# Kernel optimization log

Measured on AMD Instinct MI355X. Metric: run time of the kernel, lower is better.

Reference implementation:

```python
import jax, jax.numpy as jnp
import numpy as np
from jax import lax

B, H, W, C, G, K = 2, 64, 64, 256, 8, 9
CQ = C // 4  # PConv partial channels
HC = C // G  # head channels
PTS = np.array([[-1, -1], [-1, 0], [-1, 1], [0, -1], [0, 0], [0, 1],
                [1, -1], [1, 0], [1, 1]], np.float32)  # (K,2) as (dx,dy)


def setup_inputs() -> dict:
    key = jax.random.key(0)
    ks = jax.random.split(key, 13)
    n = lambda i, shp, s: jax.random.normal(ks[i], shp, jnp.float32) * s
    return {
        'x': jax.random.normal(ks[0], (B, H, W, C), jnp.float32),
        'qkv_w': n(1, (C, 3 * C), C ** -0.5),
        'qkv_b': n(2, (3 * C,), 0.02),
        'dw_w': n(3, (3, 3, 1, 3 * C), 1.0 / 3.0),
        'dw_b': n(4, (3 * C,), 0.02),
        'off_pconv_w': n(5, (G, CQ, CQ, 3, 3), (CQ * 9) ** -0.5),
        'off_w': n(6, (G, 2 * K, C), 0.1 * C ** -0.5),
        'off_b': n(7, (G, 2 * K), 0.1),
        'mask_pconv_w': n(8, (CQ, CQ, 3, 3), (CQ * 9) ** -0.5),
        'mask_w': n(9, (K, C), C ** -0.5),
        'mask_b': n(10, (K,), 0.02),
        'proj_w': n(11, (C, C), C ** -0.5),
        'proj_b': n(12, (C,), 0.02),
    }


def _dwconv_nhwc(x, w, b):
    # depthwise 3x3, pad 1, stride 1; x (B,H,W,ch), w (3,3,1,ch)
    ch = x.shape[-1]
    y = lax.conv_general_dilated(x, w, (1, 1), 'SAME',
                                 dimension_numbers=('NHWC', 'HWIO', 'NHWC'),
                                 feature_group_count=ch)
    return y + b


def _pconv_nchw(x, w):
    # partial conv: 3x3 (no bias) on first CQ channels, rest untouched
    dc = w.shape[0]
    x1 = lax.conv_general_dilated(x[:, :dc], w, (1, 1), 'SAME',
                                  dimension_numbers=('NCHW', 'OIHW', 'NCHW'))
    return jnp.concatenate([x1, x[:, dc:]], axis=1)


def _flow_warp(x, flow):
    # x (N,Cc,Hh,Ww), flow (N,2K,Hh,Ww) -> (N,Cc,K,Hh,Ww)
    # bilinear grid_sample, border padding, align_corners=True == sampling at
    # absolute pixel coords with coordinate clamping.
    N, Cc, Hh, Ww = x.shape
    Kk = flow.shape[1] // 2
    fl = flow.reshape(N, Kk, 2, Hh, Ww).transpose(0, 3, 4, 1, 2)  # (N,H,W,K,2)
    gy, gx = jnp.meshgrid(jnp.arange(Hh, dtype=x.dtype),
                          jnp.arange(Ww, dtype=x.dtype), indexing='ij')
    base = jnp.stack([gx, gy], axis=-1)  # (H,W,2) in (x,y) order
    coords = base[None, :, :, None, :] + fl  # (N,H,W,K,2)
    cx = jnp.clip(coords[..., 0], 0.0, Ww - 1)
    cy = jnp.clip(coords[..., 1], 0.0, Hh - 1)
    x0 = jnp.floor(cx)
    y0 = jnp.floor(cy)
    wx = (cx - x0).reshape(N, 1, -1)
    wy = (cy - y0).reshape(N, 1, -1)
    x0i = x0.astype(jnp.int32)
    y0i = y0.astype(jnp.int32)
    x1i = jnp.minimum(x0i + 1, Ww - 1)
    y1i = jnp.minimum(y0i + 1, Hh - 1)
    xf = x.reshape(N, Cc, Hh * Ww)

    def gather(yi, xi):
        idx = (yi * Ww + xi).reshape(N, -1)  # (N, H*W*K)
        return jax.vmap(lambda im, ix: im[:, ix])(xf, idx)  # (N,Cc,H*W*K)

    v00 = gather(y0i, x0i)
    v01 = gather(y0i, x1i)
    v10 = gather(y1i, x0i)
    v11 = gather(y1i, x1i)
    out = (v00 * (1 - wx) * (1 - wy) + v01 * wx * (1 - wy)
           + v10 * (1 - wx) * wy + v11 * wx * wy)
    return out.reshape(N, Cc, Hh, Ww, Kk).transpose(0, 1, 4, 2, 3)


def reference(x, qkv_w, qkv_b, dw_w, dw_b, off_pconv_w, off_w, off_b,
              mask_pconv_w, mask_w, mask_b, proj_w, proj_b):
    Bb, Hh, Ww, Cc = x.shape
    P = Hh * Ww
    scale = HC ** -0.5
    # qkv projection + depthwise conv (NHWC)
    qkv = x @ qkv_w + qkv_b                       # (B,H,W,3C)
    qkv = _dwconv_nhwc(qkv, dw_w, dw_b)
    q = qkv[..., :Cc]                             # (B,H,W,C)
    k_map = jnp.transpose(qkv[..., Cc:2 * Cc], (0, 3, 1, 2))   # (B,C,H,W)
    v_map = jnp.transpose(qkv[..., 2 * Cc:], (0, 3, 1, 2))     # (B,C,H,W)
    q_nchw = jnp.transpose(q, (0, 3, 1, 2))

    # shared mask conv: PConv + 1x1 -> (B,K,H,W)
    xm = _pconv_nchw(q_nchw, mask_pconv_w)
    mask = jnp.einsum('bchw,oc->bohw', xm, mask_w) + mask_b[None, :, None, None]

    # base offsets per group: points_pool * (2g+1), flattened (dx,dy) pairs
    base = jnp.asarray(np.stack([(PTS * (2 * g + 1)).reshape(-1)
                                 for g in range(G)], axis=0))  # (G,2K)

    k_list, v_list = [], []
    for g in range(G):
        xo = _pconv_nchw(q_nchw, off_pconv_w[g])
        off = (jnp.einsum('bchw,oc->bohw', xo, off_w[g])
               + off_b[g][None, :, None, None]
               + base[g][None, :, None, None])  # (B,2K,H,W)
        sl = slice(g * HC, (g + 1) * HC)
        k_list.append(_flow_warp(k_map[:, sl], off) * mask[:, None])
        v_list.append(_flow_warp(v_map[:, sl], off) * mask[:, None])

    # stack (G,B,hc,K,H,W) -> (B,G,P,K,hc)
    def arrange(lst):
        t = jnp.stack(lst, axis=0).transpose(1, 0, 4, 5, 3, 2)
        return t.reshape(Bb, G, P, K, HC)

    k = arrange(k_list)
    v = arrange(v_list)
    qh = (q.reshape(Bb, Hh, Ww, G, HC).transpose(0, 3, 1, 2, 4)
          .reshape(Bb, G, P, HC)) * scale

    attn = jnp.einsum('bgpc,bgpkc->bgpk', qh, k)
    attn = jax.nn.softmax(attn, axis=-1)
    out = jnp.einsum('bgpk,bgpkc->bgpc', attn, v)       # (B,G,P,hc)
    out = out.transpose(0, 2, 1, 3).reshape(Bb, Hh, Ww, Cc)
    return out @ proj_w + proj_b
```

## Files before the change

kernel.cpp:

```cpp
#include <hip/hip_runtime.h>

typedef unsigned short u16;
typedef unsigned int u32;
typedef short bf16x8 __attribute__((ext_vector_type(8)));
typedef float f32x4 __attribute__((ext_vector_type(4)));
typedef float f32x2 __attribute__((ext_vector_type(2)));

#define PP 4096
#define KPT 9

__device__ __forceinline__ u16 f2b(float f) {
    union { float f; unsigned int u; } v; v.f = f;
    unsigned int u = v.u;
    unsigned int r = u + 0x7FFFu + ((u >> 16) & 1u);
    return (u16)(r >> 16);
}
__device__ __forceinline__ float b2f(u16 b) {
    union { unsigned int u; float f; } v; v.u = ((unsigned int)b) << 16;
    return v.f;
}
__device__ __forceinline__ f32x2 unpk2(u32 u) {
    f32x2 r;
    r.x = __uint_as_float(u << 16);
    r.y = __uint_as_float(u & 0xFFFF0000u);
    return r;
}

__global__ __launch_bounds__(256) void convert_inputs(
        const float* __restrict__ qkv_w, const float* __restrict__ proj_w,
        u16* __restrict__ qkv_wT_b, u16* __restrict__ proj_wT_b) {
    int idx = blockIdx.x * 256 + threadIdx.x;
    if (idx < 196608) {
        int r = idx / 768, c = idx % 768;
        qkv_wT_b[c * 256 + r] = f2b(qkv_w[idx]);
        return;
    }
    int i3 = idx - 196608;
    int r = i3 >> 8, c = i3 & 255;
    proj_wT_b[c * 256 + r] = f2b(proj_w[i3]);
}

template<bool OUT_BF16, bool A_F32>
__global__ __launch_bounds__(256) void mfma_gemm(
        const void* __restrict__ Av, const u16* __restrict__ BT,
        const float* __restrict__ bias, void* __restrict__ out,
        int M, int N, int K) {
    __shared__ u16 As[128][40];
    __shared__ u16 Bs[64][40];
    int tid = threadIdx.x;
    int row0 = blockIdx.x * 128, col0 = blockIdx.y * 64;
    int wid = tid >> 6, lane = tid & 63;
    int wr = wid >> 1, wc = wid & 1;
    int l15 = lane & 15, lhi = lane >> 4;
    f32x4 acc[4][2] = {};
    for (int k0 = 0; k0 < K; k0 += 32) {
        #pragma unroll
        for (int q = 0; q < 2; q++) {
            int idx = tid + q * 256;
            int r = idx >> 2, kc = (idx & 3) * 8;
            if (A_F32) {
                const float* Af = (const float*)Av;
                f32x4 a0 = *(const f32x4*)&Af[(size_t)(row0 + r) * K + k0 + kc];
                f32x4 a1 = *(const f32x4*)&Af[(size_t)(row0 + r) * K + k0 + kc + 4];
                bf16x8 v;
                #pragma unroll
                for (int j = 0; j < 4; j++) { v[j] = (short)f2b(a0[j]); v[4+j] = (short)f2b(a1[j]); }
                *(bf16x8*)&As[r][kc] = v;
            } else {
                const u16* Ab = (const u16*)Av;
                *(bf16x8*)&As[r][kc] = *(const bf16x8*)&Ab[(size_t)(row0 + r) * K + k0 + kc];
            }
        }
        {
            int r = tid >> 2, kc = (tid & 3) * 8;
            *(bf16x8*)&Bs[r][kc] = *(const bf16x8*)&BT[(size_t)(col0 + r) * K + k0 + kc];
        }
        __syncthreads();
        bf16x8 bfr[2];
        #pragma unroll
        for (int j = 0; j < 2; j++)
            bfr[j] = *(const bf16x8*)&Bs[wc * 32 + j * 16 + l15][lhi * 8];
        #pragma unroll
        for (int i = 0; i < 4; i++) {
            bf16x8 afr = *(const bf16x8*)&As[wr * 64 + i * 16 + l15][lhi * 8];
            #pragma unroll
            for (int j = 0; j < 2; j++)
                acc[i][j] = __builtin_amdgcn_mfma_f32_16x16x32_bf16(afr, bfr[j], acc[i][j], 0, 0, 0);
        }
        __syncthreads();
    }
    #pragma unroll
    for (int i = 0; i < 4; i++) {
        int row = row0 + wr * 64 + i * 16 + lhi * 4;
        #pragma unroll
        for (int j = 0; j < 2; j++) {
            int col = col0 + wc * 32 + j * 16 + l15;
            float bv = bias[col];
            #pragma unroll
            for (int r = 0; r < 4; r++) {
                float v = acc[i][j][r] + bv;
                if (OUT_BF16) ((u16*)out)[(size_t)(row + r) * N + col] = f2b(v);
                else          ((float*)out)[(size_t)(row + r) * N + col] = v;
            }
        }
    }
}

__global__ __launch_bounds__(256) void dwconv_b(const u16* __restrict__ qkv_b,
        const float* __restrict__ dww, const float* __restrict__ dwb,
        u16* __restrict__ out) {
    int idx = blockIdx.x * 256 + threadIdx.x;
    int c8 = (idx % 96) * 8;
    int pix = idx / 96;
    int w = pix & 63, h = (pix >> 6) & 63, b = pix >> 12;
    float acc[8];
    #pragma unroll
    for (int j = 0; j < 8; j++) acc[j] = dwb[c8 + j];
    #pragma unroll
    for (int ky = 0; ky < 3; ky++) {
        int hh = h + ky - 1;
        if (hh < 0 || hh >= 64) continue;
        #pragma unroll
        for (int kx = 0; kx < 3; kx++) {
            int ww = w + kx - 1;
            if (ww < 0 || ww >= 64) continue;
            bf16x8 v = *(const bf16x8*)&qkv_b[((size_t)((b * 64 + hh) * 64 + ww)) * 768 + c8];
            #pragma unroll
            for (int j = 0; j < 8; j++)
                acc[j] += b2f((u16)v[j]) * dww[(ky * 3 + kx) * 768 + c8 + j];
        }
    }
    bf16x8 o;
    #pragma unroll
    for (int j = 0; j < 8; j++) o[j] = (short)f2b(acc[j]);
    *(bf16x8*)&out[(size_t)idx * 8] = o;
}

__global__ void make_cw(const float* __restrict__ off_pconv_w,
        const float* __restrict__ off_w, const float* __restrict__ off_b,
        const float* __restrict__ mask_pconv_w, const float* __restrict__ mask_w,
        const float* __restrict__ mask_b, u16* __restrict__ cwT_b,
        float* __restrict__ cb) {
    int k = blockIdx.x;
    int o = threadIdx.x;
    float val = 0.f;
    if (o < 153) {
        if (k < 576) {
            int patch = k >> 6, i = k & 63;
            if (o < 144) {
                int g = o / 18, oo = o % 18;
                for (int c = 0; c < 64; c++)
                    val += off_w[(g * 18 + oo) * 256 + c] *
                           off_pconv_w[((g * 64 + c) * 64 + i) * 9 + patch];
            } else {
                int oo = o - 144;
                for (int c = 0; c < 64; c++)
                    val += mask_w[oo * 256 + c] * mask_pconv_w[(c * 64 + i) * 9 + patch];
            }
        } else {
            int j = k - 576;
            if (o < 144) {
                int g = o / 18, oo = o % 18;
                val = off_w[(g * 18 + oo) * 256 + 64 + j];
            } else {
                val = mask_w[(o - 144) * 256 + 64 + j];
            }
        }
    }
    cwT_b[o * 768 + k] = f2b(val);
    if (k == 0) {
        float bv = 0.f;
        if (o < 144) {
            int g = o / 18, oo = o % 18;
            const float PTSf[18] = {-1,-1,-1,0,-1,1,0,-1,0,0,0,1,1,-1,1,0,1,1};
            bv = off_b[g * 18 + oo] + PTSf[oo] * (float)(2 * g + 1);
        } else if (o < 153) {
            bv = mask_b[o - 144];
        }
        cb[o] = bv;
    }
}

__global__ __launch_bounds__(256) void offmask_mfma(const u16* __restrict__ qdw_b,
        const u16* __restrict__ cwT_b, const float* __restrict__ cb,
        float* __restrict__ om0, float* __restrict__ om1) {
    __shared__ u16 As[32][40];
    __shared__ u16 Bs[160][40];
    int tid = threadIdx.x;
    int half = blockIdx.x & 1;
    int p0 = (blockIdx.x >> 1) * 32;
    int kbeg = half ? 384 : 0;
    int kend = kbeg + 384;
    int wid = tid >> 6, lane = tid & 63;
    int wr = wid >> 1, wc = wid & 1;
    int l15 = lane & 15, lhi = lane >> 4;
    f32x4 acc[5] = {};
    for (int k0 = kbeg; k0 < kend; k0 += 32) {
        if (tid < 128) {
            int r = tid >> 2, kc = (tid & 3) * 8;
            int pixel = p0 + r;
            int w = pixel & 63, h = (pixel >> 6) & 63, b = pixel >> 12;
            bf16x8 v = {};
            if (k0 < 576) {
                int patch = k0 >> 6;
                int dy = patch / 3 - 1, dx = patch % 3 - 1;
                int hh = h + dy, ww = w + dx;
                if (hh >= 0 && hh < 64 && ww >= 0 && ww < 64)
                    v = *(const bf16x8*)&qdw_b[((size_t)((b * 64 + hh) * 64 + ww)) * 768 + (k0 & 63) + kc];
            } else {
                v = *(const bf16x8*)&qdw_b[((size_t)((b * 64 + h) * 64 + w)) * 768 + 64 + (k0 - 576) + kc];
            }
            *(bf16x8*)&As[r][kc] = v;
        }
        for (int idx = tid; idx < 640; idx += 256) {
            int r = idx >> 2, kc = (idx & 3) * 8;
            *(bf16x8*)&Bs[r][kc] = *(const bf16x8*)&cwT_b[r * 768 + k0 + kc];
        }
        __syncthreads();
        bf16x8 afr = *(const bf16x8*)&As[wr * 16 + l15][lhi * 8];
        #pragma unroll
        for (int j = 0; j < 5; j++) {
            bf16x8 bfr = *(const bf16x8*)&Bs[wc * 80 + j * 16 + l15][lhi * 8];
            acc[j] = __builtin_amdgcn_mfma_f32_16x16x32_bf16(afr, bfr, acc[j], 0, 0, 0);
        }
        __syncthreads();
    }
    float* dst = half ? om1 : om0;
    int row = p0 + wr * 16 + lhi * 4;
    #pragma unroll
    for (int j = 0; j < 5; j++) {
        int col = wc * 80 + j * 16 + l15;
        float bv = half ? 0.f : cb[col];
        #pragma unroll
        for (int r = 0; r < 4; r++)
            dst[(size_t)(row + r) * 160 + col] = acc[j][r] + bv;
    }
}

__global__ __launch_bounds__(256) void precompute_pts(const float* __restrict__ om0,
        const float* __restrict__ om1, float4* __restrict__ pre) {
    int idx = blockIdx.x * 256 + threadIdx.x;
    if (idx >= 2 * PP * 72) return;
    int item = idx % 72;
    int pix = idx / 72;
    int g = item / 9, k = item % 9;
    int w = pix & 63, h = (pix >> 6) & 63;
    size_t rowb = (size_t)pix * 160;
    float dx = om0[rowb + g * 18 + 2 * k]     + om1[rowb + g * 18 + 2 * k];
    float dy = om0[rowb + g * 18 + 2 * k + 1] + om1[rowb + g * 18 + 2 * k + 1];
    float m  = om0[rowb + 144 + k]            + om1[rowb + 144 + k];
    float cx = fminf(fmaxf((float)w + dx, 0.f), 63.f);
    float cy = fminf(fmaxf((float)h + dy, 0.f), 63.f);
    float x0f = floorf(cx), y0f = floorf(cy);
    int x0 = (int)x0f, y0 = (int)y0f;
    u32 idx00 = (u32)((pix & ~4095) | (y0 << 6) | x0);
    u32 pk = idx00 | ((x0 < 63) ? 0x10000u : 0u) | ((y0 < 63) ? 0x20000u : 0u);
    float4 o;
    o.x = __uint_as_float(pk);
    o.y = cx - x0f;
    o.z = cy - y0f;
    o.w = m;
    pre[idx] = o;
}

__global__ __launch_bounds__(256) void deform_attn(const u16* __restrict__ qdw_b,
        const float4* __restrict__ pre, u16* __restrict__ attn_b) {
    int tid = threadIdx.x;
    int unit = blockIdx.x * 16 + (tid >> 4);
    int cl = tid & 15;
    int b = unit >> 15;
    int g = (unit >> 12) & 7;
    int p = unit & 4095;
    int pix = (b << 12) | p;
    const float scale = 0.17677669529663687f;
    u32 qu = *(const u32*)&qdw_b[(size_t)pix * 768 + g * 32 + 2 * cl];
    f32x2 q2 = unpk2(qu) * scale;
    const float4* pp = pre + (size_t)pix * 72 + g * 9;
    const char* base = (const char*)qdw_b;
    u32 ckb = (u32)(512 + (g * 32 + 2 * cl) * 2);
    float logit[KPT];
    f32x2 vs[KPT];
    #pragma unroll
    for (int k_ = 0; k_ < KPT; k_++) {
        float4 q4 = pp[k_];
        u32 pk = __float_as_uint(q4.x);
        float wx = q4.y, wy = q4.z, m = q4.w;
        u32 o00 = (pk & 0xFFFFu) * 1536u + ckb;
        u32 dX = (pk & 0x10000u) ? 1536u : 0u;
        u32 dY = (pk & 0x20000u) ? 98304u : 0u;
        u32 o01 = o00 + dX, o10 = o00 + dY, o11 = o00 + dY + dX;
        u32 k00 = *(const u32*)(base + o00);
        u32 v00 = *(const u32*)(base + o00 + 512);
        u32 k01 = *(const u32*)(base + o01);
        u32 v01 = *(const u32*)(base + o01 + 512);
        u32 k10 = *(const u32*)(base + o10);
        u32 v10 = *(const u32*)(base + o10 + 512);
        u32 k11 = *(const u32*)(base + o11);
        u32 v11 = *(const u32*)(base + o11 + 512);
        float w00 = (1.f - wx) * (1.f - wy), w01 = wx * (1.f - wy);
        float w10 = (1.f - wx) * wy,         w11 = wx * wy;
        f32x2 kk = unpk2(k00) * w00 + unpk2(k01) * w01
                 + unpk2(k10) * w10 + unpk2(k11) * w11;
        f32x2 vv = unpk2(v00) * w00 + unpk2(v01) * w01
                 + unpk2(v10) * w10 + unpk2(v11) * w11;
        f32x2 pr = q2 * kk;
        float part = pr.x + pr.y;
        part += __shfl_xor(part, 8);
        part += __shfl_xor(part, 4);
        part += __shfl_xor(part, 2);
        part += __shfl_xor(part, 1);
        logit[k_] = part * m;
        vs[k_] = vv * m;
    }
    float mx = logit[0];
    #pragma unroll
    for (int k_ = 1; k_ < KPT; k_++) mx = fmaxf(mx, logit[k_]);
    float s = 0.f;
    #pragma unroll
    for (int k_ = 0; k_ < KPT; k_++) { logit[k_] = expf(logit[k_] - mx); s += logit[k_]; }
    float inv = 1.f / s;
    f32x2 o2 = {0.f, 0.f};
    #pragma unroll
    for (int k_ = 0; k_ < KPT; k_++) o2 += vs[k_] * logit[k_];
    o2 *= inv;
    u32 outw = (u32)f2b(o2.x) | ((u32)f2b(o2.y) << 16);
    *(u32*)&attn_b[(size_t)pix * 256 + g * 32 + 2 * cl] = outw;
}

extern "C" void kernel_launch(void* const* d_in, const int* in_sizes, int n_in,
                              void* d_out, int out_size, void* d_ws, size_t ws_size,
                              hipStream_t stream) {
    const float* x            = (const float*)d_in[0];
    const float* qkv_w        = (const float*)d_in[1];
    const float* qkv_b        = (const float*)d_in[2];
    const float* dw_w         = (const float*)d_in[3];
    const float* dw_b         = (const float*)d_in[4];
    const float* off_pconv_w  = (const float*)d_in[5];
    const float* off_w        = (const float*)d_in[6];
    const float* off_b        = (const float*)d_in[7];
    const float* mask_pconv_w = (const float*)d_in[8];
    const float* mask_w       = (const float*)d_in[9];
    const float* mask_b       = (const float*)d_in[10];
    const float* proj_w       = (const float*)d_in[11];
    const float* proj_b       = (const float*)d_in[12];

    char* ws = (char*)d_ws;
    size_t off = 0;
    u16*   qkv_wT_b   = (u16*)(ws + off);                 off += 768ull*256*2;
    u16*   proj_wT_b  = (u16*)(ws + off);                 off += 256ull*256*2;
    u16*   qkv_bf     = (u16*)(ws + off);                 off += 8192ull*768*2;
    u16*   qdw_b      = (u16*)(ws + off);                 off += 8192ull*768*2;
    u16*   cwT_b      = (u16*)(ws + off);                 off += 160ull*768*2;
    float* cb         = (float*)(ws + off);               off += 256*4;
    float* om0        = (float*)(ws + off);               off += 8192ull*160*4;
    float* om1        = (float*)(ws + off);               off += 8192ull*160*4;
    u16*   attn_b     = (u16*)(ws + off);                 off += 8192ull*256*2;
    float4* pre       = (float4*)(ws + off);              off += 589824ull*16;

    convert_inputs<<<1024, 256, 0, stream>>>(qkv_w, proj_w, qkv_wT_b, proj_wT_b);
    make_cw<<<768, 160, 0, stream>>>(off_pconv_w, off_w, off_b,
                                     mask_pconv_w, mask_w, mask_b, cwT_b, cb);
    mfma_gemm<true, true><<<dim3(64, 12), 256, 0, stream>>>(x, qkv_wT_b, qkv_b,
                                                            qkv_bf, 8192, 768, 256);
    dwconv_b<<<3072, 256, 0, stream>>>(qkv_bf, dw_w, dw_b, qdw_b);
    offmask_mfma<<<512, 256, 0, stream>>>(qdw_b, cwT_b, cb, om0, om1);
    precompute_pts<<<2304, 256, 0, stream>>>(om0, om1, pre);
    deform_attn<<<4096, 256, 0, stream>>>(qdw_b, pre, attn_b);
    mfma_gemm<false, false><<<dim3(64, 4), 256, 0, stream>>>(attn_b, proj_wT_b, proj_b,
                                                             d_out, 8192, 256, 256);
}
```

Measured before the change: 173.2 us.

## Merge weight-prep kernels, widen deform_attn per-thread channels, template GEMM K

```diff
diff --git a/kernel.cpp b/kernel.cpp
--- a/kernel.cpp
+++ b/kernel.cpp
@@ -5,6 +5,7 @@
 typedef short bf16x8 __attribute__((ext_vector_type(8)));
 typedef float f32x4 __attribute__((ext_vector_type(4)));
 typedef float f32x2 __attribute__((ext_vector_type(2)));
+typedef u32 u32x2 __attribute__((ext_vector_type(2)));
 
 #define PP 4096
 #define KPT 9
@@ -26,123 +27,29 @@
     return r;
 }
 
-__global__ __launch_bounds__(256) void convert_inputs(
+__global__ __launch_bounds__(256) void prep_weights(
         const float* __restrict__ qkv_w, const float* __restrict__ proj_w,
-        u16* __restrict__ qkv_wT_b, u16* __restrict__ proj_wT_b) {
-    int idx = blockIdx.x * 256 + threadIdx.x;
-    if (idx < 196608) {
-        int r = idx / 768, c = idx % 768;
-        qkv_wT_b[c * 256 + r] = f2b(qkv_w[idx]);
+        const float* __restrict__ off_pconv_w, const float* __restrict__ off_w,
+        const float* __restrict__ off_b, const float* __restrict__ mask_pconv_w,
+        const float* __restrict__ mask_w, const float* __restrict__ mask_b,
+        u16* __restrict__ qkv_wT_b, u16* __restrict__ proj_wT_b,
+        u16* __restrict__ cwT_b, float* __restrict__ cb) {
+    int blk = blockIdx.x;
+    if (blk < 1024) {
+        int idx = blk * 256 + threadIdx.x;
+        if (idx < 196608) {
+            int r = idx / 768, c = idx % 768;
+            qkv_wT_b[c * 256 + r] = f2b(qkv_w[idx]);
+        } else {
+            int i3 = idx - 196608;
+            int r = i3 >> 8, c = i3 & 255;
+            proj_wT_b[c * 256 + r] = f2b(proj_w[i3]);
+        }
         return;
     }
-    int i3 = idx - 196608;
-    int r = i3 >> 8, c = i3 & 255;
-    proj_wT_b[c * 256 + r] = f2b(proj_w[i3]);
-}
-
-template<bool OUT_BF16, bool A_F32>
-__global__ __launch_bounds__(256) void mfma_gemm(
-        const void* __restrict__ Av, const u16* __restrict__ BT,
-        const float* __restrict__ bias, void* __restrict__ out,
-        int M, int N, int K) {
-    __shared__ u16 As[128][40];
-    __shared__ u16 Bs[64][40];
-    int tid = threadIdx.x;
-    int row0 = blockIdx.x * 128, col0 = blockIdx.y * 64;
-    int wid = tid >> 6, lane = tid & 63;
-    int wr = wid >> 1, wc = wid & 1;
-    int l15 = lane & 15, lhi = lane >> 4;
-    f32x4 acc[4][2] = {};
-    for (int k0 = 0; k0 < K; k0 += 32) {
-        #pragma unroll
-        for (int q = 0; q < 2; q++) {
-            int idx = tid + q * 256;
-            int r = idx >> 2, kc = (idx & 3) * 8;
-            if (A_F32) {
-                const float* Af = (const float*)Av;
-                f32x4 a0 = *(const f32x4*)&Af[(size_t)(row0 + r) * K + k0 + kc];
-                f32x4 a1 = *(const f32x4*)&Af[(size_t)(row0 + r) * K + k0 + kc + 4];
-                bf16x8 v;
-                #pragma unroll
-                for (int j = 0; j < 4; j++) { v[j] = (short)f2b(a0[j]); v[4+j] = (short)f2b(a1[j]); }
-                *(bf16x8*)&As[r][kc] = v;
-            } else {
-                const u16* Ab = (const u16*)Av;
-                *(bf16x8*)&As[r][kc] = *(const bf16x8*)&Ab[(size_t)(row0 + r) * K + k0 + kc];
-            }
-        }
-        {
-            int r = tid >> 2, kc = (tid & 3) * 8;
-            *(bf16x8*)&Bs[r][kc] = *(const bf16x8*)&BT[(size_t)(col0 + r) * K + k0 + kc];
-        }
-        __syncthreads();
-        bf16x8 bfr[2];
-        #pragma unroll
-        for (int j = 0; j < 2; j++)
-            bfr[j] = *(const bf16x8*)&Bs[wc * 32 + j * 16 + l15][lhi * 8];
-        #pragma unroll
-        for (int i = 0; i < 4; i++) {
-            bf16x8 afr = *(const bf16x8*)&As[wr * 64 + i * 16 + l15][lhi * 8];
-            #pragma unroll
-            for (int j = 0; j < 2; j++)
-                acc[i][j] = __builtin_amdgcn_mfma_f32_16x16x32_bf16(afr, bfr[j], acc[i][j], 0, 0, 0);
-        }
-        __syncthreads();
-    }
-    #pragma unroll
-    for (int i = 0; i < 4; i++) {
-        int row = row0 + wr * 64 + i * 16 + lhi * 4;
-        #pragma unroll
-        for (int j = 0; j < 2; j++) {
-            int col = col0 + wc * 32 + j * 16 + l15;
-            float bv = bias[col];
-            #pragma unroll
-            for (int r = 0; r < 4; r++) {
-                float v = acc[i][j][r] + bv;
-                if (OUT_BF16) ((u16*)out)[(size_t)(row + r) * N + col] = f2b(v);
-                else          ((float*)out)[(size_t)(row + r) * N + col] = v;
-            }
-        }
-    }
-}
-
-__global__ __launch_bounds__(256) void dwconv_b(const u16* __restrict__ qkv_b,
-        const float* __restrict__ dww, const float* __restrict__ dwb,
-        u16* __restrict__ out) {
-    int idx = blockIdx.x * 256 + threadIdx.x;
-    int c8 = (idx % 96) * 8;
-    int pix = idx / 96;
-    int w = pix & 63, h = (pix >> 6) & 63, b = pix >> 12;
-    float acc[8];
-    #pragma unroll
-    for (int j = 0; j < 8; j++) acc[j] = dwb[c8 + j];
-    #pragma unroll
-    for (int ky = 0; ky < 3; ky++) {
-        int hh = h + ky - 1;
-        if (hh < 0 || hh >= 64) continue;
-        #pragma unroll
-        for (int kx = 0; kx < 3; kx++) {
-            int ww = w + kx - 1;
-            if (ww < 0 || ww >= 64) continue;
-            bf16x8 v = *(const bf16x8*)&qkv_b[((size_t)((b * 64 + hh) * 64 + ww)) * 768 + c8];
-            #pragma unroll
-            for (int j = 0; j < 8; j++)
-                acc[j] += b2f((u16)v[j]) * dww[(ky * 3 + kx) * 768 + c8 + j];
-        }
-    }
-    bf16x8 o;
-    #pragma unroll
-    for (int j = 0; j < 8; j++) o[j] = (short)f2b(acc[j]);
-    *(bf16x8*)&out[(size_t)idx * 8] = o;
-}
-
-__global__ void make_cw(const float* __restrict__ off_pconv_w,
-        const float* __restrict__ off_w, const float* __restrict__ off_b,
-        const float* __restrict__ mask_pconv_w, const float* __restrict__ mask_w,
-        const float* __restrict__ mask_b, u16* __restrict__ cwT_b,
-        float* __restrict__ cb) {
-    int k = blockIdx.x;
+    int k = blk - 1024;
     int o = threadIdx.x;
+    if (o >= 160) return;
     float val = 0.f;
     if (o < 153) {
         if (k < 576) {
@@ -179,6 +86,102 @@
         }
         cb[o] = bv;
     }
+}
+
+template<bool OUT_BF16, bool A_F32, int KD>
+__global__ __launch_bounds__(256) void mfma_gemm(
+        const void* __restrict__ Av, const u16* __restrict__ BT,
+        const float* __restrict__ bias, void* __restrict__ out, int N) {
+    __shared__ u16 As[128][40];
+    __shared__ u16 Bs[64][40];
+    int tid = threadIdx.x;
+    int row0 = blockIdx.x * 128, col0 = blockIdx.y * 64;
+    int wid = tid >> 6, lane = tid & 63;
+    int wr = wid >> 1, wc = wid & 1;
+    int l15 = lane & 15, lhi = lane >> 4;
+    f32x4 acc[4][2] = {};
+    #pragma unroll
+    for (int k0 = 0; k0 < KD; k0 += 32) {
+        #pragma unroll
+        for (int q = 0; q < 2; q++) {
+            int idx = tid + q * 256;
+            int r = idx >> 2, kc = (idx & 3) * 8;
+            if (A_F32) {
+                const float* Af = (const float*)Av;
+                f32x4 a0 = *(const f32x4*)&Af[(size_t)(row0 + r) * KD + k0 + kc];
+                f32x4 a1 = *(const f32x4*)&Af[(size_t)(row0 + r) * KD + k0 + kc + 4];
+                bf16x8 v;
+                #pragma unroll
+                for (int j = 0; j < 4; j++) { v[j] = (short)f2b(a0[j]); v[4+j] = (short)f2b(a1[j]); }
+                *(bf16x8*)&As[r][kc] = v;
+            } else {
+                const u16* Ab = (const u16*)Av;
+                *(bf16x8*)&As[r][kc] = *(const bf16x8*)&Ab[(size_t)(row0 + r) * KD + k0 + kc];
+            }
+        }
+        {
+            int r = tid >> 2, kc = (tid & 3) * 8;
+            *(bf16x8*)&Bs[r][kc] = *(const bf16x8*)&BT[(size_t)(col0 + r) * KD + k0 + kc];
+        }
+        __syncthreads();
+        bf16x8 bfr[2];
+        #pragma unroll
+        for (int j = 0; j < 2; j++)
+            bfr[j] = *(const bf16x8*)&Bs[wc * 32 + j * 16 + l15][lhi * 8];
+        #pragma unroll
+        for (int i = 0; i < 4; i++) {
+            bf16x8 afr = *(const bf16x8*)&As[wr * 64 + i * 16 + l15][lhi * 8];
+            #pragma unroll
+            for (int j = 0; j < 2; j++)
+                acc[i][j] = __builtin_amdgcn_mfma_f32_16x16x32_bf16(afr, bfr[j], acc[i][j], 0, 0, 0);
+        }
+        __syncthreads();
+    }
+    #pragma unroll
+    for (int i = 0; i < 4; i++) {
+        int row = row0 + wr * 64 + i * 16 + lhi * 4;
+        #pragma unroll
+        for (int j = 0; j < 2; j++) {
+            int col = col0 + wc * 32 + j * 16 + l15;
+            float bv = bias[col];
+            #pragma unroll
+            for (int r = 0; r < 4; r++) {
+                float v = acc[i][j][r] + bv;
+                if (OUT_BF16) ((u16*)out)[(size_t)(row + r) * N + col] = f2b(v);
+                else          ((float*)out)[(size_t)(row + r) * N + col] = v;
+            }
+        }
+    }
+}
+
+__global__ __launch_bounds__(256) void dwconv_b(const u16* __restrict__ qkv_b,
+        const float* __restrict__ dww, const float* __restrict__ dwb,
+        u16* __restrict__ out) {
+    int idx = blockIdx.x * 256 + threadIdx.x;
+    int c8 = (idx % 96) * 8;
+    int pix = idx / 96;
+    int w = pix & 63, h = (pix >> 6) & 63, b = pix >> 12;
+    float acc[8];
+    #pragma unroll
+    for (int j = 0; j < 8; j++) acc[j] = dwb[c8 + j];
+    #pragma unroll
+    for (int ky = 0; ky < 3; ky++) {
+        int hh = h + ky - 1;
+        if (hh < 0 || hh >= 64) continue;
+        #pragma unroll
+        for (int kx = 0; kx < 3; kx++) {
+            int ww = w + kx - 1;
+            if (ww < 0 || ww >= 64) continue;
+            bf16x8 v = *(const bf16x8*)&qkv_b[((size_t)((b * 64 + hh) * 64 + ww)) * 768 + c8];
+            #pragma unroll
+            for (int j = 0; j < 8; j++)
+                acc[j] += b2f((u16)v[j]) * dww[(ky * 3 + kx) * 768 + c8 + j];
+        }
+    }
+    bf16x8 o;
+    #pragma unroll
+    for (int j = 0; j < 8; j++) o[j] = (short)f2b(acc[j]);
+    *(bf16x8*)&out[(size_t)idx * 8] = o;
 }
 
 __global__ __launch_bounds__(256) void offmask_mfma(const u16* __restrict__ qdw_b,
@@ -266,20 +269,22 @@
 __global__ __launch_bounds__(256) void deform_attn(const u16* __restrict__ qdw_b,
         const float4* __restrict__ pre, u16* __restrict__ attn_b) {
     int tid = threadIdx.x;
-    int unit = blockIdx.x * 16 + (tid >> 4);
-    int cl = tid & 15;
+    int unit = blockIdx.x * 32 + (tid >> 3);
+    int cl = tid & 7;
     int b = unit >> 15;
     int g = (unit >> 12) & 7;
     int p = unit & 4095;
     int pix = (b << 12) | p;
     const float scale = 0.17677669529663687f;
-    u32 qu = *(const u32*)&qdw_b[(size_t)pix * 768 + g * 32 + 2 * cl];
-    f32x2 q2 = unpk2(qu) * scale;
+    int c0 = g * 32 + 4 * cl;
+    u32x2 qu = *(const u32x2*)&qdw_b[(size_t)pix * 768 + c0];
+    f32x2 qa = unpk2(qu.x) * scale;
+    f32x2 qb = unpk2(qu.y) * scale;
     const float4* pp = pre + (size_t)pix * 72 + g * 9;
     const char* base = (const char*)qdw_b;
-    u32 ckb = (u32)(512 + (g * 32 + 2 * cl) * 2);
+    u32 ckb = (u32)(512 + c0 * 2);
     float logit[KPT];
-    f32x2 vs[KPT];
+    f32x2 va[KPT], vb[KPT];
     #pragma unroll
     for (int k_ = 0; k_ < KPT; k_++) {
         float4 q4 = pp[k_];
@@ -289,42 +294,48 @@
         u32 dX = (pk & 0x10000u) ? 1536u : 0u;
         u32 dY = (pk & 0x20000u) ? 98304u : 0u;
         u32 o01 = o00 + dX, o10 = o00 + dY, o11 = o00 + dY + dX;
-        u32 k00 = *(const u32*)(base + o00);
-        u32 v00 = *(const u32*)(base + o00 + 512);
-        u32 k01 = *(const u32*)(base + o01);
-        u32 v01 = *(const u32*)(base + o01 + 512);
-        u32 k10 = *(const u32*)(base + o10);
-        u32 v10 = *(const u32*)(base + o10 + 512);
-        u32 k11 = *(const u32*)(base + o11);
-        u32 v11 = *(const u32*)(base + o11 + 512);
+        u32x2 K00 = *(const u32x2*)(base + o00);
+        u32x2 V00 = *(const u32x2*)(base + o00 + 512);
+        u32x2 K01 = *(const u32x2*)(base + o01);
+        u32x2 V01 = *(const u32x2*)(base + o01 + 512);
+        u32x2 K10 = *(const u32x2*)(base + o10);
+        u32x2 V10 = *(const u32x2*)(base + o10 + 512);
+        u32x2 K11 = *(const u32x2*)(base + o11);
+        u32x2 V11 = *(const u32x2*)(base + o11 + 512);
         float w00 = (1.f - wx) * (1.f - wy), w01 = wx * (1.f - wy);
         float w10 = (1.f - wx) * wy,         w11 = wx * wy;
-        f32x2 kk = unpk2(k00) * w00 + unpk2(k01) * w01
-                 + unpk2(k10) * w10 + unpk2(k11) * w11;
-        f32x2 vv = unpk2(v00) * w00 + unpk2(v01) * w01
-                 + unpk2(v10) * w10 + unpk2(v11) * w11;
-        f32x2 pr = q2 * kk;
+        f32x2 ka = unpk2(K00.x) * w00 + unpk2(K01.x) * w01
+                 + unpk2(K10.x) * w10 + unpk2(K11.x) * w11;
+        f32x2 kb = unpk2(K00.y) * w00 + unpk2(K01.y) * w01
+                 + unpk2(K10.y) * w10 + unpk2(K11.y) * w11;
+        f32x2 vva = unpk2(V00.x) * w00 + unpk2(V01.x) * w01
+                  + unpk2(V10.x) * w10 + unpk2(V11.x) * w11;
+        f32x2 vvb = unpk2(V00.y) * w00 + unpk2(V01.y) * w01
+                  + unpk2(V10.y) * w10 + unpk2(V11.y) * w11;
+        f32x2 pr = qa * ka + qb * kb;
         float part = pr.x + pr.y;
-        part += __shfl_xor(part, 8);
         part += __shfl_xor(part, 4);
         part += __shfl_xor(part, 2);
         part += __shfl_xor(part, 1);
         logit[k_] = part * m;
-        vs[k_] = vv * m;
-    }
-    float mx = logit[0];
-    #pragma unroll
-    for (int k_ = 1; k_ < KPT; k_++) mx = fmaxf(mx, logit[k_]);
+        va[k_] = vva * m;
+        vb[k_] = vvb * m;
+    }
+    float mx = fmaxf(fmaxf(fmaxf(logit[0], logit[1]), fmaxf(logit[2], logit[3])),
+                     fmaxf(fmaxf(logit[4], logit[5]),
+                           fmaxf(fmaxf(logit[6], logit[7]), logit[8])));
     float s = 0.f;
     #pragma unroll
-    for (int k_ = 0; k_ < KPT; k_++) { logit[k_] = expf(logit[k_] - mx); s += logit[k_]; }
+    for (int k_ = 0; k_ < KPT; k_++) { logit[k_] = __expf(logit[k_] - mx); s += logit[k_]; }
     float inv = 1.f / s;
-    f32x2 o2 = {0.f, 0.f};
-    #pragma unroll
-    for (int k_ = 0; k_ < KPT; k_++) o2 += vs[k_] * logit[k_];
-    o2 *= inv;
-    u32 outw = (u32)f2b(o2.x) | ((u32)f2b(o2.y) << 16);
-    *(u32*)&attn_b[(size_t)pix * 256 + g * 32 + 2 * cl] = outw;
+    f32x2 oa = {0.f, 0.f}, ob = {0.f, 0.f};
+    #pragma unroll
+    for (int k_ = 0; k_ < KPT; k_++) { oa += va[k_] * logit[k_]; ob += vb[k_] * logit[k_]; }
+    oa *= inv; ob *= inv;
+    u32x2 outw;
+    outw.x = (u32)f2b(oa.x) | ((u32)f2b(oa.y) << 16);
+    outw.y = (u32)f2b(ob.x) | ((u32)f2b(ob.y) << 16);
+    *(u32x2*)&attn_b[(size_t)pix * 256 + c0] = outw;
 }
 
 extern "C" void kernel_launch(void* const* d_in, const int* in_sizes, int n_in,
@@ -357,15 +368,15 @@
     u16*   attn_b     = (u16*)(ws + off);                 off += 8192ull*256*2;
     float4* pre       = (float4*)(ws + off);              off += 589824ull*16;
 
-    convert_inputs<<<1024, 256, 0, stream>>>(qkv_w, proj_w, qkv_wT_b, proj_wT_b);
-    make_cw<<<768, 160, 0, stream>>>(off_pconv_w, off_w, off_b,
-                                     mask_pconv_w, mask_w, mask_b, cwT_b, cb);
-    mfma_gemm<true, true><<<dim3(64, 12), 256, 0, stream>>>(x, qkv_wT_b, qkv_b,
-                                                            qkv_bf, 8192, 768, 256);
+    prep_weights<<<1792, 256, 0, stream>>>(qkv_w, proj_w, off_pconv_w, off_w, off_b,
+                                           mask_pconv_w, mask_w, mask_b,
+                                           qkv_wT_b, proj_wT_b, cwT_b, cb);
+    mfma_gemm<true, true, 256><<<dim3(64, 12), 256, 0, stream>>>(x, qkv_wT_b, qkv_b,
+                                                                 qkv_bf, 768);
     dwconv_b<<<3072, 256, 0, stream>>>(qkv_bf, dw_w, dw_b, qdw_b);
     offmask_mfma<<<512, 256, 0, stream>>>(qdw_b, cwT_b, cb, om0, om1);
     precompute_pts<<<2304, 256, 0, stream>>>(om0, om1, pre);
-    deform_attn<<<4096, 256, 0, stream>>>(qdw_b, pre, attn_b);
-    mfma_gemm<false, false><<<dim3(64, 4), 256, 0, stream>>>(attn_b, proj_wT_b, proj_b,
-                                                             d_out, 8192, 256, 256);
-}
+    deform_attn<<<2048, 256, 0, stream>>>(qdw_b, pre, attn_b);
+    mfma_gemm<false, false, 256><<<dim3(64, 4), 256, 0, stream>>>(attn_b, proj_wT_b,
+                                                                  proj_b, d_out, 256);
+}
```

New measurement: 172.8 us. About the same (-0.3%).
